# Kernel tuning notes

Measured on AMD Instinct MI355X. Metric: run time of the kernel, lower is better.

The kernel has to match this reference:

```python
import jax, jax.numpy as jnp
import numpy as np

B, T, C, H = 8, 1024, 1024, 16
D = C // H  # head_dim = 64


def setup_inputs() -> dict:
    key = jax.random.key(0)
    k1, k2, k3 = jax.random.split(key, 3)
    x = jax.random.normal(k1, (B, T, C), dtype=jnp.float32)
    # boolean causal mask: True = attend (PyTorch SDPA bool-mask semantics)
    attn_mask = jnp.tril(jnp.ones((T, T), dtype=jnp.bool_))[None, None, :, :]
    w_attn = jax.random.normal(k2, (C, 3 * C), dtype=jnp.float32) * (1.0 / np.sqrt(C))
    b_attn = jnp.zeros((3 * C,), dtype=jnp.float32)
    w_proj = jax.random.normal(k3, (C, C), dtype=jnp.float32) * (1.0 / np.sqrt(C))
    b_proj = jnp.zeros((C,), dtype=jnp.float32)
    return {"x": x, "attn_mask": attn_mask, "w_attn": w_attn, "b_attn": b_attn,
            "w_proj": w_proj, "b_proj": b_proj}


def reference(x, attn_mask, w_attn, b_attn, w_proj, b_proj):
    Bx, Tx, Cx = x.shape
    qkv = x @ w_attn + b_attn                      # [B,T,3C]
    q, k, v = jnp.split(qkv, 3, axis=-1)
    # [B,T,C] -> [B,H,T,D]
    q = q.reshape(Bx, Tx, H, D).transpose(0, 2, 1, 3)
    k = k.reshape(Bx, Tx, H, D).transpose(0, 2, 1, 3)
    v = v.reshape(Bx, Tx, H, D).transpose(0, 2, 1, 3)
    scale = 1.0 / jnp.sqrt(jnp.asarray(D, dtype=x.dtype))
    scores = jnp.einsum('bhqd,bhkd->bhqk', q, k) * scale  # [B,H,T,T]
    neg = jnp.asarray(jnp.finfo(x.dtype).min, dtype=x.dtype)
    scores = jnp.where(attn_mask, scores, neg)
    probs = jax.nn.softmax(scores, axis=-1)
    y = jnp.einsum('bhqk,bhkd->bhqd', probs, v)    # [B,H,T,D]
    y = y.transpose(0, 2, 1, 3).reshape(Bx, Tx, Cx)
    return y @ w_proj + b_proj
```

## Files before the change

kernel.cpp:

```cpp
#include <hip/hip_runtime.h>


typedef __bf16 bf16x8 __attribute__((ext_vector_type(8)));
typedef float f32x4 __attribute__((ext_vector_type(4)));
typedef unsigned uint4e __attribute__((ext_vector_type(4)));
typedef unsigned short ushort8e __attribute__((ext_vector_type(8)));

typedef __attribute__((address_space(1))) const unsigned as1_u32;
typedef __attribute__((address_space(3))) unsigned as3_u32;

#define NEG_INF (-__builtin_inff())

__device__ __forceinline__ unsigned short f2bf(float f) {
  unsigned u = __builtin_bit_cast(unsigned, f);
  u += 0x7fffu + ((u >> 16) & 1u);
  return (unsigned short)(u >> 16);
}


__global__ void cvt_x_kernel(const float* __restrict__ in, unsigned short* __restrict__ out) {
  size_t i = (size_t)(blockIdx.x * 256 + threadIdx.x) * 8;
  float4 a = *(const float4*)(in + i);
  float4 b = *(const float4*)(in + i + 4);
  ushort8e o;
  o[0] = f2bf(a.x); o[1] = f2bf(a.y); o[2] = f2bf(a.z); o[3] = f2bf(a.w);
  o[4] = f2bf(b.x); o[5] = f2bf(b.y); o[6] = f2bf(b.z); o[7] = f2bf(b.w);
  *(ushort8e*)(out + i) = o;
}

__global__ void cvt_w_kernel(const float* __restrict__ wa, const float* __restrict__ wp,
                             unsigned short* __restrict__ wat, unsigned short* __restrict__ wpt) {
  __shared__ float tile[32][33];
  const int bx = blockIdx.x;
  const float* w; unsigned short* wT; int N, n0;
  if (bx < 96) { w = wa; wT = wat; N = 3072; n0 = bx * 32; }
  else         { w = wp; wT = wpt; N = 1024; n0 = (bx - 96) * 32; }
  const int k0 = blockIdx.y * 32;
  const int tx = threadIdx.x, ty = threadIdx.y;
#pragma unroll
  for (int i = 0; i < 32; i += 8)
    tile[ty + i][tx] = w[(size_t)(k0 + ty + i) * N + n0 + tx];
  __syncthreads();
#pragma unroll
  for (int i = 0; i < 32; i += 8)
    wT[(size_t)(n0 + ty + i) * 1024 + k0 + tx] = f2bf(tile[tx][ty + i]);
}


template <int EPI>
__device__ __forceinline__ void gemm_body(
    const unsigned short* __restrict__ A, const unsigned short* __restrict__ BT,
    const float* __restrict__ bias, void* __restrict__ out) {
  constexpr int ATILE = 256 * 64;
  constexpr int BTILE = 128 * 64;
  constexpr int NT = 16;
  constexpr int K = 1024, N = 1024;
  __shared__ __align__(16) unsigned short LDS[3][ATILE + BTILE];

  const int tid = threadIdx.x;
  const int w = tid >> 6, lane = tid & 63;
  const int g = lane >> 4, cx = lane & 15;

  const int bid = blockIdx.x;
  const int wg = (bid & 7) * 32 + (bid >> 3);
  const int bm = (wg >> 3) * 256, bn = (wg & 7) * 128;

  const int wm = (w >> 2) * 128;
  const int wn = (w & 3) * 32;

  const int srow = w * 8 + (lane >> 3);
  const int schunk = ((lane & 7) ^ ((lane >> 3) & 7)) << 3;
  const unsigned short* gAr = A + (size_t)(bm + srow) * K + schunk;
  const unsigned short* gBr = BT + (size_t)(bn + srow) * K + schunk;

  auto stage = [&](int t) {
    const int buf = t % 3;
    const int ko = t * 64;
#pragma unroll
    for (int i = 0; i < 4; ++i)
      __builtin_amdgcn_global_load_lds(
          (as1_u32*)(const void*)(gAr + (size_t)i * 64 * K + ko),
          (as3_u32*)(void*)&LDS[buf][(i * 64 + w * 8) * 64], 16, 0, 0);
#pragma unroll
    for (int i = 0; i < 2; ++i)
      __builtin_amdgcn_global_load_lds(
          (as1_u32*)(const void*)(gBr + (size_t)i * 64 * K + ko),
          (as3_u32*)(void*)&LDS[buf][ATILE + (i * 64 + w * 8) * 64], 16, 0, 0);
  };

  f32x4 acc[8][2] = {};
  const int rsw = cx & 7;

  stage(0);
  stage(1);

  for (int t = 0; t < NT; ++t) {
    if (t + 1 < NT) asm volatile("s_waitcnt vmcnt(6)" ::: "memory");
    else            asm volatile("s_waitcnt vmcnt(0)" ::: "memory");
    __builtin_amdgcn_s_barrier();
    asm volatile("" ::: "memory");
    if (t + 2 < NT) stage(t + 2);

    const unsigned short* Lb = LDS[t % 3];
    bf16x8 bfr[2][2];
#pragma unroll
    for (int nr = 0; nr < 2; ++nr) {
      const int RB = wn + nr * 16 + cx;
#pragma unroll
      for (int ks = 0; ks < 2; ++ks)
        bfr[nr][ks] = *(const bf16x8*)&Lb[ATILE + RB * 64 + (((ks * 4 + g) ^ rsw) << 3)];
    }
#pragma unroll
    for (int q = 0; q < 4; ++q) {
      bf16x8 af[2][2];
#pragma unroll
      for (int mr = 0; mr < 2; ++mr) {
        const int R = wm + q * 32 + mr * 16 + cx;
#pragma unroll
        for (int ks = 0; ks < 2; ++ks)
          af[mr][ks] = *(const bf16x8*)&Lb[R * 64 + (((ks * 4 + g) ^ rsw) << 3)];
      }
      __builtin_amdgcn_s_setprio(1);
#pragma unroll
      for (int mr = 0; mr < 2; ++mr)
#pragma unroll
        for (int nr = 0; nr < 2; ++nr)
#pragma unroll
          for (int ks = 0; ks < 2; ++ks)
            acc[q * 2 + mr][nr] = __builtin_amdgcn_mfma_f32_16x16x32_bf16(
                af[mr][ks], bfr[nr][ks], acc[q * 2 + mr][nr], 0, 0, 0);
      __builtin_amdgcn_s_setprio(0);
    }
    __builtin_amdgcn_s_barrier();
    asm volatile("" ::: "memory");
  }

#pragma unroll
  for (int q = 0; q < 4; ++q)
#pragma unroll
    for (int mr = 0; mr < 2; ++mr) {
      const int m0 = bm + wm + q * 32 + mr * 16 + (g << 2);
      const int b = m0 >> 10, t0 = m0 & 1023;
#pragma unroll
      for (int nr = 0; nr < 2; ++nr) {
        const int n = bn + wn + nr * 16 + cx;
        const float bv = bias[n];
        f32x4& a4 = acc[q * 2 + mr][nr];
        if (EPI <= 1) {
          unsigned short* dst = (unsigned short*)out;
          const int h = n >> 6, d = n & 63;
          const int bh = b * 16 + h;
          const float scl = (EPI == 0) ? 0.18033688011112042f : 1.0f;
#pragma unroll
          for (int r = 0; r < 4; ++r)
            dst[((size_t)bh * 1024 + (t0 + r)) * 64 + d] = f2bf((a4[r] + bv) * scl);
        } else if (EPI == 2) {
          unsigned short* dst = (unsigned short*)out;
          const int h = n >> 6, d = n & 63;
          const int bh = b * 16 + h;
          uint2 pv;
          pv.x = (unsigned)f2bf(a4[0] + bv) | ((unsigned)f2bf(a4[1] + bv) << 16);
          pv.y = (unsigned)f2bf(a4[2] + bv) | ((unsigned)f2bf(a4[3] + bv) << 16);
          *(uint2*)(dst + ((size_t)bh * 64 + d) * 1024 + t0) = pv;
        } else {
          float* outF = (float*)out;
#pragma unroll
          for (int r = 0; r < 4; ++r)
            outF[(size_t)(m0 + r) * N + n] = a4[r] + bv;
        }
      }
    }
}

__global__ __launch_bounds__(512, 2) void qkv_q_kernel(
    const unsigned short* __restrict__ A, const unsigned short* __restrict__ BT,
    const float* __restrict__ bias, unsigned short* __restrict__ o) {
  gemm_body<0>(A, BT, bias, o);
}
__global__ __launch_bounds__(512, 2) void qkv_k_kernel(
    const unsigned short* __restrict__ A, const unsigned short* __restrict__ BT,
    const float* __restrict__ bias, unsigned short* __restrict__ o) {
  gemm_body<1>(A, BT, bias, o);
}
__global__ __launch_bounds__(512, 2) void qkv_v_kernel(
    const unsigned short* __restrict__ A, const unsigned short* __restrict__ BT,
    const float* __restrict__ bias, unsigned short* __restrict__ o) {
  gemm_body<2>(A, BT, bias, o);
}
__global__ __launch_bounds__(512, 2) void proj_gemm_kernel(
    const unsigned short* __restrict__ A, const unsigned short* __restrict__ BT,
    const float* __restrict__ bias, float* __restrict__ o) {
  gemm_body<3>(A, BT, bias, o);
}


__global__ __launch_bounds__(256) void attn_kernel(
    const unsigned short* __restrict__ qB, const unsigned short* __restrict__ kB,
    const unsigned short* __restrict__ vB, unsigned short* __restrict__ yB) {
  __shared__ __align__(16) unsigned short Ks[2][128 * 64];
  __shared__ __align__(16) unsigned short Vs[2][64 * 128];
  const int lane = threadIdx.x & 63, w = threadIdx.x >> 6;
  const int g = lane >> 4, cx = lane & 15;
  const int bh = blockIdx.x;
  const int qt = 7 - blockIdx.y;
  const int qb0 = qt * 128;
  const int nt = qt + 1;
  const unsigned short* Qh = qB + (size_t)bh * 65536;
  const unsigned short* Kh = kB + (size_t)bh * 65536;
  const unsigned short* Vh = vB + (size_t)bh * 65536;

  const int qsb0 = qb0 + w * 16, qsb1 = qb0 + 64 + w * 16;

  bf16x8 qf[2][2];
#pragma unroll
  for (int s = 0; s < 2; ++s) {
    const int qq = (s ? qsb1 : qsb0) + cx;
#pragma unroll
    for (int h = 0; h < 2; ++h)
      qf[s][h] = *(const bf16x8*)(Qh + (size_t)qq * 64 + h * 32 + g * 8);
  }

  f32x4 oacc[2][4] = {};
  float L0 = 0.f, L1 = 0.f;

  auto stage = [&](int t, int buf) {
#pragma unroll
    for (int i = 0; i < 4; ++i) {
      const int row = i * 32 + w * 8 + (lane >> 3);
      const int csw = ((lane & 7) ^ (row & 7)) << 3;
      __builtin_amdgcn_global_load_lds(
          (as1_u32*)(const void*)(Kh + (size_t)(t * 128 + row) * 64 + csw),
          (as3_u32*)(void*)&Ks[buf][(i * 32 + w * 8) * 64], 16, 0, 0);
    }
#pragma unroll
    for (int i = 0; i < 4; ++i) {
      const int d = w * 16 + i * 4 + (lane >> 4);
      const int gc = ((lane & 15) ^ (d & 7)) << 3;
      __builtin_amdgcn_global_load_lds(
          (as1_u32*)(const void*)(Vh + (size_t)d * 1024 + t * 128 + gc),
          (as3_u32*)(void*)&Vs[buf][(w * 16 + i * 4) * 128], 16, 0, 0);
    }
  };

  auto cvtpk = [](float lo, float hi) -> unsigned {
    unsigned r;
    asm("v_cvt_pk_bf16_f32 %0, %1, %2" : "=v"(r) : "v"(lo), "v"(hi));
    return r;
  };

  auto mkpf = [&](const float* pp) -> bf16x8 {
    unsigned lo0 = cvtpk(pp[0], pp[1]);
    unsigned hi0 = cvtpk(pp[2], pp[3]);
    unsigned lo1 = cvtpk(pp[4], pp[5]);
    unsigned hi1 = cvtpk(pp[6], pp[7]);
    const int s0 = ((g & 1) << 5) + cx, s1 = s0 + 16;
    unsigned a0 = __shfl(lo0, s0), a1 = __shfl(hi0, s0), a2 = __shfl(lo0, s1), a3 = __shfl(hi0, s1);
    unsigned b0 = __shfl(lo1, s0), b1 = __shfl(hi1, s0), b2 = __shfl(lo1, s1), b3 = __shfl(hi1, s1);
    const bool chh = g >= 2;
    uint4e pw;
    pw[0] = chh ? b0 : a0; pw[1] = chh ? b1 : a1; pw[2] = chh ? b2 : a2; pw[3] = chh ? b3 : a3;
    return __builtin_bit_cast(bf16x8, pw);
  };

  stage(0, 0);
  asm volatile("s_waitcnt vmcnt(0)" ::: "memory");
  __builtin_amdgcn_s_barrier();
  asm volatile("" ::: "memory");

  for (int t = 0; t < nt; ++t) {
    const int buf = t & 1;
    if (t + 1 < nt) stage(t + 1, buf ^ 1);

#pragma unroll
    for (int half = 0; half < 2; ++half) {
      const int k0 = t * 128 + half * 64;
      const bool act0 = k0 <= qsb0 + 15;

      bf16x8 kf[4][2];
#pragma unroll
      for (int kc = 0; kc < 4; ++kc) {
        const int row = half * 64 + kc * 16 + cx;
#pragma unroll
        for (int h = 0; h < 2; ++h)
          kf[kc][h] = *(const bf16x8*)&Ks[buf][row * 64 + (((h * 4 + g) ^ (row & 7)) << 3)];
      }
      f32x4 sa[2][4];
      __builtin_amdgcn_s_setprio(1);
#pragma unroll
      for (int kc = 0; kc < 4; ++kc) {
        f32x4 z = {0.f, 0.f, 0.f, 0.f};
        sa[1][kc] = __builtin_amdgcn_mfma_f32_16x16x32_bf16(kf[kc][0], qf[1][0], z, 0, 0, 0);
        sa[1][kc] = __builtin_amdgcn_mfma_f32_16x16x32_bf16(kf[kc][1], qf[1][1], sa[1][kc], 0, 0, 0);
      }
      if (act0) {
#pragma unroll
        for (int kc = 0; kc < 4; ++kc) {
          f32x4 z = {0.f, 0.f, 0.f, 0.f};
          sa[0][kc] = __builtin_amdgcn_mfma_f32_16x16x32_bf16(kf[kc][0], qf[0][0], z, 0, 0, 0);
          sa[0][kc] = __builtin_amdgcn_mfma_f32_16x16x32_bf16(kf[kc][1], qf[0][1], sa[0][kc], 0, 0, 0);
        }
      }
      __builtin_amdgcn_s_setprio(0);

      bf16x8 vf[4][2];
#pragma unroll
      for (int db = 0; db < 4; ++db) {
        const int d = db * 16 + cx;
#pragma unroll
        for (int ks = 0; ks < 2; ++ks) {
          const int c16 = half * 8 + ks * 4 + g;
          vf[db][ks] = *(const bf16x8*)&Vs[buf][d * 128 + ((c16 ^ (d & 7)) << 3)];
        }
      }

#pragma unroll
      for (int s = 0; s < 2; ++s) {
        if (s == 0 && !act0) continue;
        const int qsb = s ? qsb1 : qsb0;
        const int qg = qsb + cx;
        float& L = s ? L1 : L0;
        float p[16];
        const bool straddle = (k0 + 63) > qsb;
#pragma unroll
        for (int kc = 0; kc < 4; ++kc)
#pragma unroll
          for (int r = 0; r < 4; ++r) {
            float v = sa[s][kc][r];
            if (straddle && (k0 + kc * 16 + (g << 2) + r) > qg) v = NEG_INF;
            p[kc * 4 + r] = v;
          }
        float ps = 0.f;
#pragma unroll
        for (int e = 0; e < 16; ++e) {
          p[e] = __builtin_amdgcn_exp2f(p[e]);
          ps += p[e];
        }
        L += ps;
        const bf16x8 pf0 = mkpf(p);
        const bf16x8 pf1 = mkpf(p + 8);
        __builtin_amdgcn_s_setprio(1);
#pragma unroll
        for (int db = 0; db < 4; ++db) {
          oacc[s][db] = __builtin_amdgcn_mfma_f32_16x16x32_bf16(vf[db][0], pf0, oacc[s][db], 0, 0, 0);
          oacc[s][db] = __builtin_amdgcn_mfma_f32_16x16x32_bf16(vf[db][1], pf1, oacc[s][db], 0, 0, 0);
        }
        __builtin_amdgcn_s_setprio(0);
      }
    }

    asm volatile("s_waitcnt vmcnt(0)" ::: "memory");
    __builtin_amdgcn_s_barrier();
    asm volatile("" ::: "memory");
  }

  const int b = bh >> 4, h = bh & 15;
#pragma unroll
  for (int s = 0; s < 2; ++s) {
    float Lt = s ? L1 : L0;
    Lt += __shfl_xor(Lt, 16);
    Lt += __shfl_xor(Lt, 32);
    const float inv = 1.0f / Lt;
    const int qg = (s ? qsb1 : qsb0) + cx;
    unsigned short* yp = yB + (size_t)(b * 1024 + qg) * 1024 + h * 64;
#pragma unroll
    for (int db = 0; db < 4; ++db) {
      uint2 pv;
      pv.x = (unsigned)f2bf(oacc[s][db][0] * inv) | ((unsigned)f2bf(oacc[s][db][1] * inv) << 16);
      pv.y = (unsigned)f2bf(oacc[s][db][2] * inv) | ((unsigned)f2bf(oacc[s][db][3] * inv) << 16);
      *(uint2*)(yp + db * 16 + (g << 2)) = pv;
    }
  }
}


extern "C" void kernel_launch(void* const* d_in, const int* in_sizes, int n_in,
                              void* d_out, int out_size, void* d_ws, size_t ws_size,
                              hipStream_t stream) {
  (void)in_sizes; (void)n_in; (void)out_size; (void)ws_size;
  const float* x = (const float*)d_in[0];
  const float* w_attn = (const float*)d_in[2];
  const float* b_attn = (const float*)d_in[3];
  const float* w_proj = (const float*)d_in[4];
  const float* b_proj = (const float*)d_in[5];
  float* out = (float*)d_out;

  char* ws = (char*)d_ws;
  unsigned short* xb     = (unsigned short*)(ws);
  unsigned short* wqkvT  = (unsigned short*)(ws + 16777216);
  unsigned short* wprojT = (unsigned short*)(ws + 23068672);
  unsigned short* qb     = (unsigned short*)(ws + 25165824);
  unsigned short* kb     = (unsigned short*)(ws + 41943040);
  unsigned short* vtb    = (unsigned short*)(ws + 58720256);
  unsigned short* yb     = (unsigned short*)(ws + 75497472);

  cvt_x_kernel<<<4096, 256, 0, stream>>>(x, xb);
  cvt_w_kernel<<<dim3(128, 32), dim3(32, 8), 0, stream>>>(w_attn, w_proj, wqkvT, wprojT);

  qkv_q_kernel<<<256, 512, 0, stream>>>(xb, wqkvT,                 b_attn,        qb);
  qkv_k_kernel<<<256, 512, 0, stream>>>(xb, wqkvT + 1024 * 1024,   b_attn + 1024, kb);
  qkv_v_kernel<<<256, 512, 0, stream>>>(xb, wqkvT + 2048 * 1024,   b_attn + 2048, vtb);
  attn_kernel<<<dim3(128, 8), 256, 0, stream>>>(qb, kb, vtb, yb);
  proj_gemm_kernel<<<256, 512, 0, stream>>>(yb, wprojT, b_proj, out);
}
```

Measured before the change: 145.9 us.

## Merge conversion and QKV launches, retile GEMMs to 128x128 with BK=32

Merges the x and weight conversion kernels into one launch, and merges the three QKV GEMM launches into one 1536-block kernel that picks its Q/K/V slice from the block index. The GEMM tile shrinks from 256x128 with 512 threads and BK=64 to 128x128 with 256 threads and BK=32, using a new LDS swizzle and 3 blocks per CU. The goal is to cut launch overhead, fill the CUs better, and overlap work across slices. The trade-off is less reuse per tile and twice as many K iterations and barriers.

```diff
diff --git a/kernel.cpp b/kernel.cpp
--- a/kernel.cpp
+++ b/kernel.cpp
@@ -18,25 +18,29 @@
 }
 
 
-__global__ void cvt_x_kernel(const float* __restrict__ in, unsigned short* __restrict__ out) {
-  size_t i = (size_t)(blockIdx.x * 256 + threadIdx.x) * 8;
-  float4 a = *(const float4*)(in + i);
-  float4 b = *(const float4*)(in + i + 4);
-  ushort8e o;
-  o[0] = f2bf(a.x); o[1] = f2bf(a.y); o[2] = f2bf(a.z); o[3] = f2bf(a.w);
-  o[4] = f2bf(b.x); o[5] = f2bf(b.y); o[6] = f2bf(b.z); o[7] = f2bf(b.w);
-  *(ushort8e*)(out + i) = o;
-}
-
-__global__ void cvt_w_kernel(const float* __restrict__ wa, const float* __restrict__ wp,
-                             unsigned short* __restrict__ wat, unsigned short* __restrict__ wpt) {
+__global__ void cvt_all_kernel(const float* __restrict__ xin, unsigned short* __restrict__ xout,
+                               const float* __restrict__ wa, const float* __restrict__ wp,
+                               unsigned short* __restrict__ wat, unsigned short* __restrict__ wpt) {
   __shared__ float tile[32][33];
   const int bx = blockIdx.x;
+  const int tid = threadIdx.x;
+  if (bx < 4096) {
+    size_t i = (size_t)(bx * 256 + tid) * 8;
+    float4 a = *(const float4*)(xin + i);
+    float4 b = *(const float4*)(xin + i + 4);
+    ushort8e o;
+    o[0] = f2bf(a.x); o[1] = f2bf(a.y); o[2] = f2bf(a.z); o[3] = f2bf(a.w);
+    o[4] = f2bf(b.x); o[5] = f2bf(b.y); o[6] = f2bf(b.z); o[7] = f2bf(b.w);
+    *(ushort8e*)(xout + i) = o;
+    return;
+  }
+  const int wb = bx - 4096;
+  const int nb = wb & 127, kb = wb >> 7;
   const float* w; unsigned short* wT; int N, n0;
-  if (bx < 96) { w = wa; wT = wat; N = 3072; n0 = bx * 32; }
-  else         { w = wp; wT = wpt; N = 1024; n0 = (bx - 96) * 32; }
-  const int k0 = blockIdx.y * 32;
-  const int tx = threadIdx.x, ty = threadIdx.y;
+  if (nb < 96) { w = wa; wT = wat; N = 3072; n0 = nb * 32; }
+  else         { w = wp; wT = wpt; N = 1024; n0 = (nb - 96) * 32; }
+  const int k0 = kb * 32;
+  const int tx = tid & 31, ty = tid >> 5;
 #pragma unroll
   for (int i = 0; i < 32; i += 8)
     tile[ty + i][tx] = w[(size_t)(k0 + ty + i) * N + n0 + tx];
@@ -50,147 +54,117 @@
 template <int EPI>
 __device__ __forceinline__ void gemm_body(
     const unsigned short* __restrict__ A, const unsigned short* __restrict__ BT,
-    const float* __restrict__ bias, void* __restrict__ out) {
-  constexpr int ATILE = 256 * 64;
-  constexpr int BTILE = 128 * 64;
-  constexpr int NT = 16;
-  constexpr int K = 1024, N = 1024;
-  __shared__ __align__(16) unsigned short LDS[3][ATILE + BTILE];
+    const float* __restrict__ bias, void* __restrict__ o0,
+    unsigned short* __restrict__ kO, unsigned short* __restrict__ vO, int slice) {
+  constexpr int ATILE = 128 * 32;
+  constexpr int NT = 32;
+  constexpr int K = 1024;
+  __shared__ __align__(16) unsigned short LDS[3][2 * ATILE];
 
   const int tid = threadIdx.x;
   const int w = tid >> 6, lane = tid & 63;
   const int g = lane >> 4, cx = lane & 15;
 
-  const int bid = blockIdx.x;
-  const int wg = (bid & 7) * 32 + (bid >> 3);
-  const int bm = (wg >> 3) * 256, bn = (wg & 7) * 128;
-
-  const int wm = (w >> 2) * 128;
-  const int wn = (w & 3) * 32;
-
-  const int srow = w * 8 + (lane >> 3);
-  const int schunk = ((lane & 7) ^ ((lane >> 3) & 7)) << 3;
-  const unsigned short* gAr = A + (size_t)(bm + srow) * K + schunk;
-  const unsigned short* gBr = BT + (size_t)(bn + srow) * K + schunk;
-
+  const int bid = blockIdx.x & 511;
+  const int wg = (bid & 7) * 64 + (bid >> 3);
+  const int bm = (wg >> 3) * 128, bn = (wg & 7) * 128;
+
+  const int wm = (w >> 1) * 64, wn = (w & 1) * 64;
+
+  const int srow0 = w * 16 + (lane >> 2);
   auto stage = [&](int t) {
     const int buf = t % 3;
-    const int ko = t * 64;
-#pragma unroll
-    for (int i = 0; i < 4; ++i)
+    const int ko = t * 32;
+#pragma unroll
+    for (int i = 0; i < 2; ++i) {
+      const int row = i * 64 + srow0;
+      const int csw = (((lane & 3) ^ ((row >> 1) & 3)) << 3);
       __builtin_amdgcn_global_load_lds(
-          (as1_u32*)(const void*)(gAr + (size_t)i * 64 * K + ko),
-          (as3_u32*)(void*)&LDS[buf][(i * 64 + w * 8) * 64], 16, 0, 0);
-#pragma unroll
-    for (int i = 0; i < 2; ++i)
+          (as1_u32*)(const void*)(A + (size_t)(bm + row) * K + ko + csw),
+          (as3_u32*)(void*)&LDS[buf][(i * 64 + w * 16) * 32], 16, 0, 0);
       __builtin_amdgcn_global_load_lds(
-          (as1_u32*)(const void*)(gBr + (size_t)i * 64 * K + ko),
-          (as3_u32*)(void*)&LDS[buf][ATILE + (i * 64 + w * 8) * 64], 16, 0, 0);
+          (as1_u32*)(const void*)(BT + (size_t)(bn + row) * K + ko + csw),
+          (as3_u32*)(void*)&LDS[buf][ATILE + (i * 64 + w * 16) * 32], 16, 0, 0);
+    }
   };
 
-  f32x4 acc[8][2] = {};
-  const int rsw = cx & 7;
+  f32x4 acc[4][4] = {};
 
   stage(0);
   stage(1);
 
   for (int t = 0; t < NT; ++t) {
-    if (t + 1 < NT) asm volatile("s_waitcnt vmcnt(6)" ::: "memory");
+    if (t + 1 < NT) asm volatile("s_waitcnt vmcnt(4)" ::: "memory");
     else            asm volatile("s_waitcnt vmcnt(0)" ::: "memory");
     __builtin_amdgcn_s_barrier();
     asm volatile("" ::: "memory");
     if (t + 2 < NT) stage(t + 2);
 
     const unsigned short* Lb = LDS[t % 3];
-    bf16x8 bfr[2][2];
-#pragma unroll
-    for (int nr = 0; nr < 2; ++nr) {
-      const int RB = wn + nr * 16 + cx;
-#pragma unroll
-      for (int ks = 0; ks < 2; ++ks)
-        bfr[nr][ks] = *(const bf16x8*)&Lb[ATILE + RB * 64 + (((ks * 4 + g) ^ rsw) << 3)];
-    }
-#pragma unroll
-    for (int q = 0; q < 4; ++q) {
-      bf16x8 af[2][2];
-#pragma unroll
-      for (int mr = 0; mr < 2; ++mr) {
-        const int R = wm + q * 32 + mr * 16 + cx;
-#pragma unroll
-        for (int ks = 0; ks < 2; ++ks)
-          af[mr][ks] = *(const bf16x8*)&Lb[R * 64 + (((ks * 4 + g) ^ rsw) << 3)];
-      }
-      __builtin_amdgcn_s_setprio(1);
-#pragma unroll
-      for (int mr = 0; mr < 2; ++mr)
-#pragma unroll
-        for (int nr = 0; nr < 2; ++nr)
-#pragma unroll
-          for (int ks = 0; ks < 2; ++ks)
-            acc[q * 2 + mr][nr] = __builtin_amdgcn_mfma_f32_16x16x32_bf16(
-                af[mr][ks], bfr[nr][ks], acc[q * 2 + mr][nr], 0, 0, 0);
-      __builtin_amdgcn_s_setprio(0);
-    }
+    bf16x8 af[4], bfr[4];
+#pragma unroll
+    for (int i = 0; i < 4; ++i) {
+      const int R = wm + i * 16 + cx;
+      af[i] = *(const bf16x8*)&Lb[R * 32 + ((g ^ ((R >> 1) & 3)) << 3)];
+      const int Rb = wn + i * 16 + cx;
+      bfr[i] = *(const bf16x8*)&Lb[ATILE + Rb * 32 + ((g ^ ((Rb >> 1) & 3)) << 3)];
+    }
+    __builtin_amdgcn_s_setprio(1);
+#pragma unroll
+    for (int i = 0; i < 4; ++i)
+#pragma unroll
+      for (int j = 0; j < 4; ++j)
+        acc[i][j] = __builtin_amdgcn_mfma_f32_16x16x32_bf16(af[i], bfr[j], acc[i][j], 0, 0, 0);
+    __builtin_amdgcn_s_setprio(0);
     __builtin_amdgcn_s_barrier();
     asm volatile("" ::: "memory");
   }
 
 #pragma unroll
-  for (int q = 0; q < 4; ++q)
-#pragma unroll
-    for (int mr = 0; mr < 2; ++mr) {
-      const int m0 = bm + wm + q * 32 + mr * 16 + (g << 2);
-      const int b = m0 >> 10, t0 = m0 & 1023;
-#pragma unroll
-      for (int nr = 0; nr < 2; ++nr) {
-        const int n = bn + wn + nr * 16 + cx;
-        const float bv = bias[n];
-        f32x4& a4 = acc[q * 2 + mr][nr];
-        if (EPI <= 1) {
-          unsigned short* dst = (unsigned short*)out;
-          const int h = n >> 6, d = n & 63;
-          const int bh = b * 16 + h;
-          const float scl = (EPI == 0) ? 0.18033688011112042f : 1.0f;
-#pragma unroll
-          for (int r = 0; r < 4; ++r)
-            dst[((size_t)bh * 1024 + (t0 + r)) * 64 + d] = f2bf((a4[r] + bv) * scl);
-        } else if (EPI == 2) {
-          unsigned short* dst = (unsigned short*)out;
-          const int h = n >> 6, d = n & 63;
-          const int bh = b * 16 + h;
+  for (int i = 0; i < 4; ++i) {
+    const int m0 = bm + wm + i * 16 + (g << 2);
+    const int b = m0 >> 10, t0 = m0 & 1023;
+#pragma unroll
+    for (int j = 0; j < 4; ++j) {
+      const int n = bn + wn + j * 16 + cx;
+      const float bv = bias[n];
+      f32x4& a4 = acc[i][j];
+      if (EPI == 1) {
+        float* outF = (float*)o0;
+#pragma unroll
+        for (int r = 0; r < 4; ++r)
+          outF[(size_t)(m0 + r) * 1024 + n] = a4[r] + bv;
+      } else {
+        const int h = n >> 6, d = n & 63;
+        const int bh = b * 16 + h;
+        if (slice == 2) {
           uint2 pv;
           pv.x = (unsigned)f2bf(a4[0] + bv) | ((unsigned)f2bf(a4[1] + bv) << 16);
           pv.y = (unsigned)f2bf(a4[2] + bv) | ((unsigned)f2bf(a4[3] + bv) << 16);
-          *(uint2*)(dst + ((size_t)bh * 64 + d) * 1024 + t0) = pv;
+          *(uint2*)(vO + ((size_t)bh * 64 + d) * 1024 + t0) = pv;
         } else {
-          float* outF = (float*)out;
+          unsigned short* dst = (slice == 0) ? (unsigned short*)o0 : kO;
+          const float scl = (slice == 0) ? 0.18033688011112042f : 1.0f;
 #pragma unroll
           for (int r = 0; r < 4; ++r)
-            outF[(size_t)(m0 + r) * N + n] = a4[r] + bv;
-        }
-      }
-    }
-}
-
-__global__ __launch_bounds__(512, 2) void qkv_q_kernel(
+            dst[((size_t)bh * 1024 + (t0 + r)) * 64 + d] = f2bf((a4[r] + bv) * scl);
+        }
+      }
+    }
+  }
+}
+
+__global__ __launch_bounds__(256, 3) void qkv_gemm_kernel(
+    const unsigned short* __restrict__ A, const unsigned short* __restrict__ BT0,
+    const float* __restrict__ bias0, unsigned short* __restrict__ qO,
+    unsigned short* __restrict__ kO, unsigned short* __restrict__ vO) {
+  const int slice = blockIdx.x >> 9;
+  gemm_body<0>(A, BT0 + ((size_t)slice << 20), bias0 + slice * 1024, qO, kO, vO, slice);
+}
+__global__ __launch_bounds__(256, 3) void proj_gemm_kernel(
     const unsigned short* __restrict__ A, const unsigned short* __restrict__ BT,
-    const float* __restrict__ bias, unsigned short* __restrict__ o) {
-  gemm_body<0>(A, BT, bias, o);
-}
-__global__ __launch_bounds__(512, 2) void qkv_k_kernel(
-    const unsigned short* __restrict__ A, const unsigned short* __restrict__ BT,
-    const float* __restrict__ bias, unsigned short* __restrict__ o) {
-  gemm_body<1>(A, BT, bias, o);
-}
-__global__ __launch_bounds__(512, 2) void qkv_v_kernel(
-    const unsigned short* __restrict__ A, const unsigned short* __restrict__ BT,
-    const float* __restrict__ bias, unsigned short* __restrict__ o) {
-  gemm_body<2>(A, BT, bias, o);
-}
-__global__ __launch_bounds__(512, 2) void proj_gemm_kernel(
-    const unsigned short* __restrict__ A, const unsigned short* __restrict__ BT,
-    const float* __restrict__ bias, float* __restrict__ o) {
-  gemm_body<3>(A, BT, bias, o);
+    const float* __restrict__ bias, float* __restrict__ outF) {
+  gemm_body<1>(A, BT, bias, outF, nullptr, nullptr, 0);
 }
 
 
@@ -393,12 +367,8 @@
   unsigned short* vtb    = (unsigned short*)(ws + 58720256);
   unsigned short* yb     = (unsigned short*)(ws + 75497472);
 
-  cvt_x_kernel<<<4096, 256, 0, stream>>>(x, xb);
-  cvt_w_kernel<<<dim3(128, 32), dim3(32, 8), 0, stream>>>(w_attn, w_proj, wqkvT, wprojT);
-
-  qkv_q_kernel<<<256, 512, 0, stream>>>(xb, wqkvT,                 b_attn,        qb);
-  qkv_k_kernel<<<256, 512, 0, stream>>>(xb, wqkvT + 1024 * 1024,   b_attn + 1024, kb);
-  qkv_v_kernel<<<256, 512, 0, stream>>>(xb, wqkvT + 2048 * 1024,   b_attn + 2048, vtb);
+  cvt_all_kernel<<<8192, 256, 0, stream>>>(x, xb, w_attn, w_proj, wqkvT, wprojT);
+  qkv_gemm_kernel<<<1536, 256, 0, stream>>>(xb, wqkvT, b_attn, qb, kb, vtb);
   attn_kernel<<<dim3(128, 8), 256, 0, stream>>>(qb, kb, vtb, yb);
-  proj_gemm_kernel<<<256, 512, 0, stream>>>(yb, wprojT, b_proj, out);
-}
+  proj_gemm_kernel<<<512, 256, 0, stream>>>(yb, wprojT, b_proj, out);
+}
```

Result: no change. 144.2 us (-1.2%).
